# Performance work log

Hardware: AMD Instinct MI355X
Metric: run time of the kernel (lower is better)

## Reference

```python
import jax, jax.numpy as jnp
import numpy as np

B, S, H, E, K = 4, 2048, 1024, 8, 2
DFF = H * 8 // 3  # 2730, as in up: Linear(H, H*8//3)


def setup_inputs() -> dict:
    key = jax.random.key(0)
    ks = jax.random.split(key, 6)
    s = lambda fan: 1.0 / np.sqrt(fan)
    return {
        "x": jax.random.normal(ks[0], (B, S, H), jnp.float32),
        "Wr": jax.random.normal(ks[1], (H, E), jnp.float32) * s(H),
        "br": jnp.zeros((E,), jnp.float32),
        "Wg": jax.random.normal(ks[2], (E, H, H), jnp.float32) * s(H),
        "bg": jnp.zeros((E, H), jnp.float32),
        "Wu": jax.random.normal(ks[3], (E, H, DFF), jnp.float32) * s(H),
        "bu": jnp.zeros((E, DFF), jnp.float32),
        "Wd": jax.random.normal(ks[4], (E, DFF, H), jnp.float32) * s(DFF),
        "bd": jnp.zeros((E, H), jnp.float32),
    }


def reference(x, Wr, br, Wg, bg, Wu, bu, Wd, bd):
    b, s_, h = x.shape
    n = b * s_
    # Router: logits -> softmax -> top-k -> renormalize top-k weights
    expert_weight = x @ Wr + br                      # [B,S,E] (returned raw logits)
    logits_flat = expert_weight.reshape(n, -1)       # [N,E]
    probs = jax.nn.softmax(logits_flat, axis=-1)
    w, idx = jax.lax.top_k(probs, K)                 # [N,K]
    w = w / w.sum(axis=-1, keepdims=True)
    # Scatter top-k weights into dense [N,E] combine matrix (zeros elsewhere)
    rw = jnp.zeros_like(logits_flat).at[jnp.arange(n)[:, None], idx].add(w)
    # Expert MLP (BasicExpert): down(silu(up(gate(x)))); dropout is identity at eval
    xf = x.reshape(n, h)                             # [N,H]
    g = jnp.einsum("nh,ehf->enf", xf, Wg) + bg[:, None, :]       # [E,N,H]
    u = jax.nn.silu(jnp.einsum("enf,efd->end", g, Wu) + bu[:, None, :])  # [E,N,DFF]
    d = jnp.einsum("end,edh->enh", u, Wd) + bd[:, None, :]       # [E,N,H]
    # Combine: weighted sum over experts (weight is 0 for non-selected experts)
    y = jnp.einsum("enh,ne->nh", d, rw)
    return y.reshape(b, s_, h), expert_weight
```

## Files before the change

kernel.cpp:

```cpp
#include <hip/hip_runtime.h>
#include <hip/hip_bf16.h>

#define NB 4
#define SS 2048
#define HH 1024
#define EE 8
#define KK 2
#define DFF 2730
#define DFFP 2752
#define NT (NB*SS)
#define NA (NT*KK)
#define YSZ ((size_t)NT*HH)

using bf16x8 = __attribute__((ext_vector_type(8))) short;
using f32x4  = __attribute__((ext_vector_type(4))) float;

__device__ __forceinline__ ushort f2bf(float f) {
  unsigned u = __float_as_uint(f);
  unsigned r = (u + 0x7FFFu + ((u >> 16) & 1u)) >> 16;
  return (ushort)r;
}

__device__ __forceinline__ void gload16(const ushort* g, ushort* s) {
  __builtin_amdgcn_global_load_lds((const __attribute__((address_space(1))) void*)g,
                                   (__attribute__((address_space(3))) void*)s, 16, 0, 0);
}

__global__ __launch_bounds__(256) void transpose_cvt_kernel(
    const float* __restrict__ in, ushort* __restrict__ out,
    int K, int Nn, int Kpad, int Nnpad, long in_estride, long out_estride) {
  __shared__ float t[64][65];
  int e = blockIdx.z;
  const float* ine = in + (size_t)e * in_estride;
  ushort* oute = out + (size_t)e * out_estride;
  int nb = blockIdx.x * 64, kb = blockIdx.y * 64;
  int tid = threadIdx.x;
  int rr = tid >> 4, cc = (tid & 15) * 4;
  if (kb + 64 <= K && nb + 64 <= Nn) {
#pragma unroll
    for (int i = 0; i < 4; ++i) {
      int r = rr + i * 16;
      const float* src = ine + (size_t)(kb + r) * Nn + nb + cc;
      float2 a = *(const float2*)src;
      float2 b = *(const float2*)(src + 2);
      t[r][cc] = a.x; t[r][cc + 1] = a.y; t[r][cc + 2] = b.x; t[r][cc + 3] = b.y;
    }
  } else {
#pragma unroll
    for (int i = 0; i < 4; ++i) {
      int r = rr + i * 16;
      int kg = kb + r;
#pragma unroll
      for (int j = 0; j < 4; ++j) {
        int ng = nb + cc + j;
        t[r][cc + j] = (kg < K && ng < Nn) ? ine[(size_t)kg * Nn + ng] : 0.0f;
      }
    }
  }
  __syncthreads();
  int kq = tid & 15;
#pragma unroll
  for (int i = 0; i < 4; ++i) {
    int nl = rr + i * 16, ng = nb + nl;
    ushort4 v;
    v.x = f2bf(t[kq * 4 + 0][nl]);
    v.y = f2bf(t[kq * 4 + 1][nl]);
    v.z = f2bf(t[kq * 4 + 2][nl]);
    v.w = f2bf(t[kq * 4 + 3][nl]);
    *(ushort4*)&oute[(size_t)ng * Kpad + kb + kq * 4] = v;
  }
}

__global__ __launch_bounds__(256) void router_kernel(
    const float* __restrict__ x, const float* __restrict__ Wr, const float* __restrict__ br,
    float* __restrict__ logits_out, int* __restrict__ counts,
    int* __restrict__ tok_e, float* __restrict__ tok_w, ushort* __restrict__ xb) {
  int wv = threadIdx.x >> 6, l = threadIdx.x & 63;
  int n = blockIdx.x * 4 + wv;
  const float* xr = x + (size_t)n * HH;
  ushort* xbr = xb + (size_t)n * HH;
  float acc[8] = {0, 0, 0, 0, 0, 0, 0, 0};
#pragma unroll 4
  for (int i = 0; i < 16; ++i) {
    int k = l + i * 64;
    float xv = xr[k];
    xbr[k] = f2bf(xv);
    const float4* w4 = (const float4*)(Wr + (size_t)k * 8);
    float4 a = w4[0], b = w4[1];
    acc[0] += xv * a.x; acc[1] += xv * a.y; acc[2] += xv * a.z; acc[3] += xv * a.w;
    acc[4] += xv * b.x; acc[5] += xv * b.y; acc[6] += xv * b.z; acc[7] += xv * b.w;
  }
#pragma unroll
  for (int s = 1; s < 64; s <<= 1)
#pragma unroll
    for (int e2 = 0; e2 < 8; ++e2) acc[e2] += __shfl_xor(acc[e2], s);
#pragma unroll
  for (int e2 = 0; e2 < 8; ++e2) acc[e2] += br[e2];
  if (l < 8) logits_out[(size_t)n * 8 + l] = acc[l];
  if (l == 0) {
    int i0 = 0;
#pragma unroll
    for (int e2 = 1; e2 < 8; ++e2) if (acc[e2] > acc[i0]) i0 = e2;
    int i1 = (i0 == 0) ? 1 : 0;
#pragma unroll
    for (int e2 = 0; e2 < 8; ++e2) if (e2 != i0 && acc[e2] > acc[i1]) i1 = e2;
    float e10 = __expf(acc[i1] - acc[i0]);
    float w0 = 1.0f / (1.0f + e10);
    tok_e[2 * n] = i0; tok_e[2 * n + 1] = i1;
    tok_w[2 * n] = w0; tok_w[2 * n + 1] = e10 / (1.0f + e10);
    atomicAdd(&counts[i0], 1); atomicAdd(&counts[i1], 1);
  }
}

__global__ void prefix_kernel(const int* __restrict__ counts, int* __restrict__ bases,
                              int* __restrict__ cursor) {
  if (threadIdx.x == 0) {
    int s = 0;
    for (int e = 0; e < EE; ++e) { bases[e] = s; s += counts[e]; }
    bases[EE] = s;
  }
  if (threadIdx.x < EE) cursor[threadIdx.x] = 0;
}

__global__ __launch_bounds__(256) void scatter_kernel(
    const int* __restrict__ tok_e, const float* __restrict__ tok_w,
    const int* __restrict__ bases, int* __restrict__ cursor,
    int* __restrict__ assign_token, float* __restrict__ assign_w) {
  int n = blockIdx.x * 256 + threadIdx.x;
  if (n >= NT) return;
#pragma unroll
  for (int k2 = 0; k2 < 2; ++k2) {
    int e = tok_e[2 * n + k2];
    int pos = atomicAdd(&cursor[e], 1);
    int slot = bases[e] + pos;
    assign_token[slot] = n;
    assign_w[slot] = tok_w[2 * n + k2];
  }
}

template <int MODE, int MB, int NBT>
__global__ __launch_bounds__(256, 2) void moe_gemm_kernel(
    const ushort* __restrict__ Abase, const ushort* __restrict__ Wbase,
    const float* __restrict__ bias, ushort* __restrict__ outb, float* __restrict__ y,
    const int* __restrict__ bases, const int* __restrict__ assign_token,
    const float* __restrict__ assign_w,
    int K, int lda, long wstride_e, int bias_stride, int ldc,
    int ncols_valid, int ncols_write, int wrows) {
  constexpr int nwg = MB * NBT * EE;
  constexpr int q = nwg >> 3, r8 = nwg & 7;
  int orig = blockIdx.x;
  int xcd = orig & 7, pos = orig >> 3;
  int id = (xcd < r8 ? xcd * (q + 1) : r8 * (q + 1) + (xcd - r8) * q) + pos;
  int m = id % MB; int t2 = id / MB;
  int n = t2 % NBT;
  int e = t2 / NBT;

  int base = bases[e], Ce = bases[e + 1] - base;
  int m0 = m * 128;
  if (m0 >= Ce) return;
  int n0 = n * 128;
  int rows_valid = Ce - m0; if (rows_valid > 128) rows_valid = 128;

  __shared__ ushort lds[32768];
  int tid = threadIdx.x, w = tid >> 6, l = tid & 63;
  int wm = w >> 1, wn = w & 1;

  const ushort* aptr[4];
  const ushort* bptr[4];
  int lofs[4];
  const ushort* We = Wbase + (size_t)e * wstride_e;
#pragma unroll
  for (int i = 0; i < 4; ++i) {
    int s = i * 4 + w;
    int chunk = s * 64 + l;
    int r = chunk >> 3, cir = chunk & 7;
    int cirs = cir ^ (r & 7);
    int ar = r < rows_valid ? r : rows_valid - 1;
    int slot = base + m0 + ar;
    long arow = (MODE == 0) ? (long)assign_token[slot] : (long)slot;
    aptr[i] = Abase + arow * (long)lda + cirs * 8;
    int wr = n0 + r; if (wr >= wrows) wr = wrows - 1;
    bptr[i] = We + (size_t)wr * K + cirs * 8;
    lofs[i] = s * 512;
  }

  f32x4 acc[4][4];
#pragma unroll
  for (int a1 = 0; a1 < 4; ++a1)
#pragma unroll
    for (int b1 = 0; b1 < 4; ++b1) acc[a1][b1] = f32x4{0.f, 0.f, 0.f, 0.f};

  int nk = K >> 6;
#pragma unroll
  for (int i = 0; i < 4; ++i) {
    gload16(aptr[i], &lds[lofs[i]]);
    gload16(bptr[i], &lds[8192 + lofs[i]]);
  }
  asm volatile("s_waitcnt vmcnt(0)" ::: "memory");
  __builtin_amdgcn_s_barrier();

  int cur = 0;
  for (int t = 0; t < nk; ++t) {
    int nxt = cur ^ 1;
    if (t + 1 < nk) {
      int k0 = (t + 1) << 6;
#pragma unroll
      for (int i = 0; i < 4; ++i) {
        gload16(aptr[i] + k0, &lds[nxt * 16384 + lofs[i]]);
        gload16(bptr[i] + k0, &lds[nxt * 16384 + 8192 + lofs[i]]);
      }
    }
    const ushort* cA = &lds[cur * 16384];
    const ushort* cB = &lds[cur * 16384 + 8192];
#pragma unroll
    for (int ks = 0; ks < 2; ++ks) {
      bf16x8 af[4], bfr[4];
#pragma unroll
      for (int mt = 0; mt < 4; ++mt) {
        int row = wm * 64 + mt * 16 + (l & 15);
        int cir = (ks * 4 + (l >> 4)) ^ (row & 7);
        af[mt] = *(const bf16x8*)&cA[row * 64 + cir * 8];
      }
#pragma unroll
      for (int nt = 0; nt < 4; ++nt) {
        int row = wn * 64 + nt * 16 + (l & 15);
        int cir = (ks * 4 + (l >> 4)) ^ (row & 7);
        bfr[nt] = *(const bf16x8*)&cB[row * 64 + cir * 8];
      }
      __builtin_amdgcn_s_setprio(1);
#pragma unroll
      for (int mt = 0; mt < 4; ++mt)
#pragma unroll
        for (int nt = 0; nt < 4; ++nt)
          acc[mt][nt] = __builtin_amdgcn_mfma_f32_16x16x32_bf16(af[mt], bfr[nt], acc[mt][nt], 0, 0, 0);
      __builtin_amdgcn_s_setprio(0);
    }
    asm volatile("s_waitcnt vmcnt(0)" ::: "memory");
    __builtin_amdgcn_s_barrier();
    cur = nxt;
  }

  int lr = l >> 4, lc = l & 15;
#pragma unroll
  for (int mt = 0; mt < 4; ++mt) {
#pragma unroll
    for (int i2 = 0; i2 < 4; ++i2) {
      int r = wm * 64 + mt * 16 + lr * 4 + i2;
      if (r >= rows_valid) continue;
      int slot = base + m0 + r;
      int tok = 0; float wgt = 0.f;
      if (MODE == 2) { tok = assign_token[slot]; wgt = assign_w[slot]; }
#pragma unroll
      for (int nt = 0; nt < 4; ++nt) {
        int col = n0 + wn * 64 + nt * 16 + lc;
        if (col >= ncols_write) continue;
        float v = acc[mt][nt][i2];
        if (MODE == 0) {
          v += bias[e * bias_stride + col];
          outb[(size_t)slot * ldc + col] = f2bf(v);
        } else if (MODE == 1) {
          float o = 0.0f;
          if (col < ncols_valid) {
            v += bias[e * bias_stride + col];
            o = v / (1.0f + __expf(-v));
          }
          outb[(size_t)slot * ldc + col] = f2bf(o);
        } else {
          v += bias[e * bias_stride + col];
          atomicAdd(&y[(size_t)tok * HH + col], wgt * v);
        }
      }
    }
  }
}

extern "C" void kernel_launch(void* const* d_in, const int* in_sizes, int n_in,
                              void* d_out, int out_size, void* d_ws, size_t ws_size,
                              hipStream_t stream) {
  const float* x  = (const float*)d_in[0];
  const float* Wr = (const float*)d_in[1];
  const float* br = (const float*)d_in[2];
  const float* Wg = (const float*)d_in[3];
  const float* bg = (const float*)d_in[4];
  const float* Wu = (const float*)d_in[5];
  const float* bu = (const float*)d_in[6];
  const float* Wd = (const float*)d_in[7];
  const float* bd = (const float*)d_in[8];
  float* y = (float*)d_out;
  float* logits = y + YSZ;

  char* ws = (char*)d_ws;
  size_t o = 0;
  auto alloc = [&](size_t b) { size_t r = o; o = (o + b + 255) & ~(size_t)255; return r; };
  size_t XB  = alloc((size_t)NT * HH * 2);
  size_t WGT = alloc((size_t)EE * HH * HH * 2);
  size_t WUT = alloc((size_t)EE * DFFP * HH * 2);
  size_t WDT = alloc((size_t)EE * HH * DFFP * 2);
  size_t G   = alloc((size_t)NA * HH * 2);
  size_t U   = alloc((size_t)NA * DFFP * 2);
  size_t META = alloc(262400);

  ushort* xb  = (ushort*)(ws + XB);
  ushort* wgt = (ushort*)(ws + WGT);
  ushort* wut = (ushort*)(ws + WUT);
  ushort* wdt = (ushort*)(ws + WDT);
  ushort* g   = (ushort*)(ws + G);
  ushort* u   = (ushort*)(ws + U);
  int* meta = (int*)(ws + META);
  int* counts = meta;
  int* bases  = meta + 16;
  int* cursor = meta + 32;
  int* tok_e  = meta + 64;
  float* tok_w = (float*)(tok_e + NA);
  int* assign_token = (int*)(tok_w + NA);
  float* assign_w = (float*)(assign_token + NA);

  hipMemsetAsync(y, 0, YSZ * sizeof(float), stream);
  hipMemsetAsync(meta, 0, 256, stream);

  router_kernel<<<NT / 4, 256, 0, stream>>>(x, Wr, br, logits, counts, tok_e, tok_w, xb);
  transpose_cvt_kernel<<<dim3(16, 16, EE), 256, 0, stream>>>(Wg, wgt, HH, HH, HH, HH,
                                                             (long)HH * HH, (long)HH * HH);
  transpose_cvt_kernel<<<dim3(DFFP / 64, 16, EE), 256, 0, stream>>>(Wu, wut, HH, DFF, HH, DFFP,
                                                                    (long)HH * DFF, (long)DFFP * HH);
  transpose_cvt_kernel<<<dim3(16, DFFP / 64, EE), 256, 0, stream>>>(Wd, wdt, DFF, HH, DFFP, HH,
                                                                    (long)DFF * HH, (long)HH * DFFP);
  prefix_kernel<<<1, 64, 0, stream>>>(counts, bases, cursor);
  scatter_kernel<<<NT / 256, 256, 0, stream>>>(tok_e, tok_w, bases, cursor, assign_token, assign_w);

  moe_gemm_kernel<0, 17, 8><<<17 * 8 * EE, 256, 0, stream>>>(
      xb, wgt, bg, g, nullptr, bases, assign_token, assign_w,
      HH, HH, (long)HH * HH, HH, HH, HH, HH, HH);
  moe_gemm_kernel<1, 17, 22><<<17 * 22 * EE, 256, 0, stream>>>(
      g, wut, bu, u, nullptr, bases, assign_token, assign_w,
      HH, HH, (long)DFFP * HH, DFF, DFFP, DFF, DFFP, DFFP);
  moe_gemm_kernel<2, 17, 8><<<17 * 8 * EE, 256, 0, stream>>>(
      u, wdt, bd, nullptr, y, bases, assign_token, assign_w,
      DFFP, DFFP, (long)HH * DFFP, HH, HH, HH, HH, HH);
}
```

Measured before the change: 862.6 us.

## Add 256x256-tile MoE GEMM kernel with split-K for up and down projections

Introduces a new 512-thread GEMM kernel using 256x256 output tiles with XCD-aware block remapping. The up projection and the down projection (split-K by 2, bias added only in the first chunk) now use it. The aim is more data reuse per tile and fewer redundant weight loads. The costs are higher register and LDS pressure, more padding waste on partial expert tiles, and doubled atomic traffic for the down projection. The original kernel is simplified to serve only the gate projection.

```diff
diff --git a/kernel.cpp b/kernel.cpp
--- a/kernel.cpp
+++ b/kernel.cpp
@@ -248,6 +248,125 @@
       int r = wm * 64 + mt * 16 + lr * 4 + i2;
       if (r >= rows_valid) continue;
       int slot = base + m0 + r;
+#pragma unroll
+      for (int nt = 0; nt < 4; ++nt) {
+        int col = n0 + wn * 64 + nt * 16 + lc;
+        if (col >= ncols_write) continue;
+        float v = acc[mt][nt][i2] + bias[e * bias_stride + col];
+        outb[(size_t)slot * ldc + col] = f2bf(v);
+      }
+    }
+  }
+}
+
+template <int MODE, int MB, int NBT, int KS>
+__global__ __launch_bounds__(512, 2) void moe_gemm_256(
+    const ushort* __restrict__ Abase, const ushort* __restrict__ Wbase,
+    const float* __restrict__ bias, ushort* __restrict__ outb, float* __restrict__ y,
+    const int* __restrict__ bases, const int* __restrict__ assign_token,
+    const float* __restrict__ assign_w,
+    int K, int lda, long wstride_e, int bias_stride, int ldc,
+    int ncols_valid, int ncols_write, int wrows) {
+  constexpr int nwg = MB * NBT * KS * EE;
+  constexpr int q = nwg >> 3, r8 = nwg & 7;
+  int orig = blockIdx.x;
+  int xcd = orig & 7, pos = orig >> 3;
+  int id = (xcd < r8 ? xcd * (q + 1) : r8 * (q + 1) + (xcd - r8) * q) + pos;
+  int m = id % MB; id /= MB;
+  int n = id % NBT; id /= NBT;
+  int kc = (KS > 1) ? (id % KS) : 0;
+  int e = (KS > 1) ? (id / KS) : id;
+
+  int base = bases[e], Ce = bases[e + 1] - base;
+  int m0 = m * 256;
+  if (m0 >= Ce) return;
+  int n0 = n * 256;
+  int rows_valid = Ce - m0; if (rows_valid > 256) rows_valid = 256;
+  int kch = K / KS;
+  int k_begin = kc * kch;
+
+  __shared__ ushort lds[32768];
+  int tid = threadIdx.x, w = tid >> 6, l = tid & 63;
+  int wm = w >> 2, wn = w & 3;
+
+  const ushort* aptr[2];
+  const ushort* bptr[2];
+  int lofs[2];
+  const ushort* We = Wbase + (size_t)e * wstride_e;
+  int csrc = ((l & 3) ^ ((l >> 3) & 3)) * 8;
+#pragma unroll
+  for (int i = 0; i < 2; ++i) {
+    int r = i * 128 + w * 16 + (l >> 2);
+    int ar = r < rows_valid ? r : rows_valid - 1;
+    long arow = (long)(base + m0 + ar);
+    aptr[i] = Abase + arow * (long)lda + k_begin + csrc;
+    int wr = n0 + r; if (wr >= wrows) wr = wrows - 1;
+    bptr[i] = We + (size_t)wr * K + k_begin + csrc;
+    lofs[i] = (i * 512 + w * 64) * 8;
+  }
+
+  f32x4 acc[8][4];
+#pragma unroll
+  for (int a1 = 0; a1 < 8; ++a1)
+#pragma unroll
+    for (int b1 = 0; b1 < 4; ++b1) acc[a1][b1] = f32x4{0.f, 0.f, 0.f, 0.f};
+
+  int nk = kch >> 5;
+#pragma unroll
+  for (int i = 0; i < 2; ++i) {
+    gload16(aptr[i], &lds[lofs[i]]);
+    gload16(bptr[i], &lds[8192 + lofs[i]]);
+  }
+  asm volatile("s_waitcnt vmcnt(0)" ::: "memory");
+  __builtin_amdgcn_s_barrier();
+
+  int l15 = l & 15, g4 = l >> 4;
+  int cur = 0;
+  for (int t = 0; t < nk; ++t) {
+    int nxt = cur ^ 1;
+    if (t + 1 < nk) {
+      int k0 = (t + 1) << 5;
+#pragma unroll
+      for (int i = 0; i < 2; ++i) {
+        gload16(aptr[i] + k0, &lds[nxt * 16384 + lofs[i]]);
+        gload16(bptr[i] + k0, &lds[nxt * 16384 + 8192 + lofs[i]]);
+      }
+    }
+    const ushort* cA = &lds[cur * 16384];
+    const ushort* cB = &lds[cur * 16384 + 8192];
+    bf16x8 af[8], bfr[4];
+#pragma unroll
+    for (int mt = 0; mt < 8; ++mt) {
+      int row = wm * 128 + mt * 16 + l15;
+      int cir = g4 ^ ((row >> 1) & 3);
+      af[mt] = *(const bf16x8*)&cA[row * 32 + cir * 8];
+    }
+#pragma unroll
+    for (int nt = 0; nt < 4; ++nt) {
+      int row = wn * 64 + nt * 16 + l15;
+      int cir = g4 ^ ((row >> 1) & 3);
+      bfr[nt] = *(const bf16x8*)&cB[row * 32 + cir * 8];
+    }
+    __builtin_amdgcn_s_setprio(1);
+#pragma unroll
+    for (int mt = 0; mt < 8; ++mt)
+#pragma unroll
+      for (int nt = 0; nt < 4; ++nt)
+        acc[mt][nt] = __builtin_amdgcn_mfma_f32_16x16x32_bf16(af[mt], bfr[nt], acc[mt][nt], 0, 0, 0);
+    __builtin_amdgcn_s_setprio(0);
+    asm volatile("s_waitcnt vmcnt(0)" ::: "memory");
+    __builtin_amdgcn_s_barrier();
+    cur = nxt;
+  }
+
+  int lr = l >> 4, lc = l & 15;
+#pragma unroll
+  for (int mt = 0; mt < 8; ++mt) {
+#pragma unroll
+    for (int i2 = 0; i2 < 4; ++i2) {
+      int r = wm * 128 + mt * 16 + lr * 4 + i2;
+      if (r >= rows_valid) continue;
+      int slot = base + m0 + r;
       int tok = 0; float wgt = 0.f;
       if (MODE == 2) { tok = assign_token[slot]; wgt = assign_w[slot]; }
 #pragma unroll
@@ -255,10 +374,7 @@
         int col = n0 + wn * 64 + nt * 16 + lc;
         if (col >= ncols_write) continue;
         float v = acc[mt][nt][i2];
-        if (MODE == 0) {
-          v += bias[e * bias_stride + col];
-          outb[(size_t)slot * ldc + col] = f2bf(v);
-        } else if (MODE == 1) {
+        if (MODE == 1) {
           float o = 0.0f;
           if (col < ncols_valid) {
             v += bias[e * bias_stride + col];
@@ -266,7 +382,7 @@
           }
           outb[(size_t)slot * ldc + col] = f2bf(o);
         } else {
-          v += bias[e * bias_stride + col];
+          if (kc == 0) v += bias[e * bias_stride + col];
           atomicAdd(&y[(size_t)tok * HH + col], wgt * v);
         }
       }
@@ -331,10 +447,10 @@
   moe_gemm_kernel<0, 17, 8><<<17 * 8 * EE, 256, 0, stream>>>(
       xb, wgt, bg, g, nullptr, bases, assign_token, assign_w,
       HH, HH, (long)HH * HH, HH, HH, HH, HH, HH);
-  moe_gemm_kernel<1, 17, 22><<<17 * 22 * EE, 256, 0, stream>>>(
+  moe_gemm_256<1, 9, 11, 1><<<9 * 11 * EE, 512, 0, stream>>>(
       g, wut, bu, u, nullptr, bases, assign_token, assign_w,
       HH, HH, (long)DFFP * HH, DFF, DFFP, DFF, DFFP, DFFP);
-  moe_gemm_kernel<2, 17, 8><<<17 * 8 * EE, 256, 0, stream>>>(
+  moe_gemm_256<2, 9, 4, 2><<<9 * 4 * 2 * EE, 512, 0, stream>>>(
       u, wdt, bd, nullptr, y, bases, assign_token, assign_w,
       DFFP, DFFP, (long)HH * DFFP, HH, HH, HH, HH, HH);
 }
```

After: 916.9 us. +6.3%, slower.

## Fold gate and up projections into a single precomputed combined weight per expert

Applied to the files above, without the earlier changes.

Since there is no nonlinearity between the gate and up projections, the code multiplies the up weights by the gate weights per expert to form one combined bf16 weight and a combined bias. The token-side gate GEMM and its intermediate buffer are removed, so tokens go straight from x to the up output. In exchange, a weight-by-weight GEMM over all experts runs every call, which is roughly as much arithmetic as the removed per-token GEMM, and rounding the product to bf16 changes numerics.

```diff
diff --git a/kernel.cpp b/kernel.cpp
--- a/kernel.cpp
+++ b/kernel.cpp
@@ -24,6 +24,16 @@
 __device__ __forceinline__ void gload16(const ushort* g, ushort* s) {
   __builtin_amdgcn_global_load_lds((const __attribute__((address_space(1))) void*)g,
                                    (__attribute__((address_space(3))) void*)s, 16, 0, 0);
+}
+
+__global__ __launch_bounds__(256) void cvt_w_kernel(const float4* __restrict__ in4,
+                                                    ushort4* __restrict__ o4, int n4) {
+  int i = blockIdx.x * 256 + threadIdx.x;
+  if (i >= n4) return;
+  float4 v = in4[i];
+  ushort4 o;
+  o.x = f2bf(v.x); o.y = f2bf(v.y); o.z = f2bf(v.z); o.w = f2bf(v.w);
+  o4[i] = o;
 }
 
 __global__ __launch_bounds__(256) void transpose_cvt_kernel(
@@ -138,6 +148,30 @@
   }
 }
 
+__global__ __launch_bounds__(256) void bcomb_kernel(
+    const ushort* __restrict__ wut, const float* __restrict__ bg,
+    const float* __restrict__ bu, float* __restrict__ bc) {
+  int gid = blockIdx.x * 4 + (threadIdx.x >> 6);
+  int l = threadIdx.x & 63;
+  int e = gid / DFFP, d = gid - e * DFFP;
+  const ushort* row = wut + ((size_t)e * DFFP + d) * HH;
+  const float* bge = bg + (size_t)e * HH;
+  float s = 0.f;
+#pragma unroll
+  for (int i = 0; i < 4; ++i) {
+    int k = (l + i * 64) * 4;
+    ushort4 w4 = *(const ushort4*)&row[k];
+    float4 b4 = *(const float4*)&bge[k];
+    s += __uint_as_float((unsigned)w4.x << 16) * b4.x
+       + __uint_as_float((unsigned)w4.y << 16) * b4.y
+       + __uint_as_float((unsigned)w4.z << 16) * b4.z
+       + __uint_as_float((unsigned)w4.w << 16) * b4.w;
+  }
+#pragma unroll
+  for (int sh = 1; sh < 64; sh <<= 1) s += __shfl_xor(s, sh);
+  if (l == 0) bc[(size_t)e * DFFP + d] = s + ((d < DFF) ? bu[(size_t)e * DFF + d] : 0.f);
+}
+
 template <int MODE, int MB, int NBT>
 __global__ __launch_bounds__(256, 2) void moe_gemm_kernel(
     const ushort* __restrict__ Abase, const ushort* __restrict__ Wbase,
@@ -155,7 +189,9 @@
   int n = t2 % NBT;
   int e = t2 / NBT;
 
-  int base = bases[e], Ce = bases[e + 1] - base;
+  int base, Ce;
+  if (MODE == 3) { base = e * DFFP; Ce = DFFP; }
+  else           { base = bases[e]; Ce = bases[e + 1] - base; }
   int m0 = m * 128;
   if (m0 >= Ce) return;
   int n0 = n * 128;
@@ -177,7 +213,7 @@
     int cirs = cir ^ (r & 7);
     int ar = r < rows_valid ? r : rows_valid - 1;
     int slot = base + m0 + ar;
-    long arow = (MODE == 0) ? (long)assign_token[slot] : (long)slot;
+    long arow = (MODE == 4) ? (long)assign_token[slot] : (long)slot;
     aptr[i] = Abase + arow * (long)lda + cirs * 8;
     int wr = n0 + r; if (wr >= wrows) wr = wrows - 1;
     bptr[i] = We + (size_t)wr * K + cirs * 8;
@@ -255,18 +291,17 @@
         int col = n0 + wn * 64 + nt * 16 + lc;
         if (col >= ncols_write) continue;
         float v = acc[mt][nt][i2];
-        if (MODE == 0) {
-          v += bias[e * bias_stride + col];
+        if (MODE == 3) {
           outb[(size_t)slot * ldc + col] = f2bf(v);
-        } else if (MODE == 1) {
+        } else if (MODE == 4) {
           float o = 0.0f;
           if (col < ncols_valid) {
-            v += bias[e * bias_stride + col];
+            v += bias[(size_t)e * bias_stride + col];
             o = v / (1.0f + __expf(-v));
           }
           outb[(size_t)slot * ldc + col] = f2bf(o);
         } else {
-          v += bias[e * bias_stride + col];
+          v += bias[(size_t)e * bias_stride + col];
           atomicAdd(&y[(size_t)tok * HH + col], wgt * v);
         }
       }
@@ -293,19 +328,21 @@
   size_t o = 0;
   auto alloc = [&](size_t b) { size_t r = o; o = (o + b + 255) & ~(size_t)255; return r; };
   size_t XB  = alloc((size_t)NT * HH * 2);
-  size_t WGT = alloc((size_t)EE * HH * HH * 2);
+  size_t WGN = alloc((size_t)EE * HH * HH * 2);
   size_t WUT = alloc((size_t)EE * DFFP * HH * 2);
   size_t WDT = alloc((size_t)EE * HH * DFFP * 2);
-  size_t G   = alloc((size_t)NA * HH * 2);
+  size_t WCB = alloc((size_t)EE * DFFP * HH * 2);
   size_t U   = alloc((size_t)NA * DFFP * 2);
+  size_t BC  = alloc((size_t)EE * DFFP * 4);
   size_t META = alloc(262400);
 
   ushort* xb  = (ushort*)(ws + XB);
-  ushort* wgt = (ushort*)(ws + WGT);
+  ushort* wgn = (ushort*)(ws + WGN);
   ushort* wut = (ushort*)(ws + WUT);
   ushort* wdt = (ushort*)(ws + WDT);
-  ushort* g   = (ushort*)(ws + G);
+  ushort* wcb = (ushort*)(ws + WCB);
   ushort* u   = (ushort*)(ws + U);
+  float* bcomb = (float*)(ws + BC);
   int* meta = (int*)(ws + META);
   int* counts = meta;
   int* bases  = meta + 16;
@@ -319,21 +356,22 @@
   hipMemsetAsync(meta, 0, 256, stream);
 
   router_kernel<<<NT / 4, 256, 0, stream>>>(x, Wr, br, logits, counts, tok_e, tok_w, xb);
-  transpose_cvt_kernel<<<dim3(16, 16, EE), 256, 0, stream>>>(Wg, wgt, HH, HH, HH, HH,
-                                                             (long)HH * HH, (long)HH * HH);
+  cvt_w_kernel<<<(EE * HH * HH / 4 + 255) / 256, 256, 0, stream>>>(
+      (const float4*)Wg, (ushort4*)wgn, EE * HH * HH / 4);
   transpose_cvt_kernel<<<dim3(DFFP / 64, 16, EE), 256, 0, stream>>>(Wu, wut, HH, DFF, HH, DFFP,
                                                                     (long)HH * DFF, (long)DFFP * HH);
   transpose_cvt_kernel<<<dim3(16, DFFP / 64, EE), 256, 0, stream>>>(Wd, wdt, DFF, HH, DFFP, HH,
                                                                     (long)DFF * HH, (long)HH * DFFP);
   prefix_kernel<<<1, 64, 0, stream>>>(counts, bases, cursor);
   scatter_kernel<<<NT / 256, 256, 0, stream>>>(tok_e, tok_w, bases, cursor, assign_token, assign_w);
-
-  moe_gemm_kernel<0, 17, 8><<<17 * 8 * EE, 256, 0, stream>>>(
-      xb, wgt, bg, g, nullptr, bases, assign_token, assign_w,
-      HH, HH, (long)HH * HH, HH, HH, HH, HH, HH);
-  moe_gemm_kernel<1, 17, 22><<<17 * 22 * EE, 256, 0, stream>>>(
-      g, wut, bu, u, nullptr, bases, assign_token, assign_w,
-      HH, HH, (long)DFFP * HH, DFF, DFFP, DFF, DFFP, DFFP);
+  bcomb_kernel<<<EE * DFFP / 4, 256, 0, stream>>>(wut, bg, bu, bcomb);
+
+  moe_gemm_kernel<3, 22, 8><<<22 * 8 * EE, 256, 0, stream>>>(
+      wut, wgn, nullptr, wcb, nullptr, nullptr, nullptr, nullptr,
+      HH, HH, (long)HH * HH, 0, HH, HH, HH, HH);
+  moe_gemm_kernel<4, 17, 22><<<17 * 22 * EE, 256, 0, stream>>>(
+      xb, wcb, bcomb, u, nullptr, bases, assign_token, nullptr,
+      HH, HH, (long)DFFP * HH, DFFP, DFFP, DFF, DFFP, DFFP);
   moe_gemm_kernel<2, 17, 8><<<17 * 8 * EE, 256, 0, stream>>>(
       u, wdt, bd, nullptr, y, bases, assign_token, assign_w,
       DFFP, DFFP, (long)HH * DFFP, HH, HH, HH, HH, HH);
```

New measurement: 844.6 us. 2.1% less time.
